# Kernel optimization log

Measured on AMD Instinct MI355X. Metric: run time of the kernel, lower is better.

## Reference

```python
import jax, jax.numpy as jnp
import numpy as np

B, C, T, F_ = 4, 128, 1000, 65
H, E, Dh = 4, 8, 32          # E = ceil(512/65), Dh = C // H
POOL, STRIDE = 10, 5
EPS = 1e-5


def setup_inputs() -> dict:
    key = jax.random.key(0)
    ks = jax.random.split(key, 16)
    s = 0.05
    d = {}
    d['batch'] = jax.random.normal(ks[0], (B, C, T, F_), jnp.float32)
    d['pos_cond'] = jax.random.normal(ks[1], (B, C, T, F_), jnp.float32)
    d['neg_cond'] = jax.random.normal(ks[2], (B, C, T, F_), jnp.float32)
    # per-head 1x1 conv params (stacked over heads), PReLU slopes, LN4DCF affine
    d['WQ'] = jax.random.normal(ks[3], (H, E, C), jnp.float32) * s
    d['bQ'] = jax.random.normal(ks[4], (H, E), jnp.float32) * s
    d['aQ'] = jnp.full((H,), 0.25, jnp.float32)
    d['gQ'] = jnp.ones((H, E, F_), jnp.float32)
    d['betQ'] = jnp.zeros((H, E, F_), jnp.float32)
    d['WK'] = jax.random.normal(ks[5], (H, E, C), jnp.float32) * s
    d['bK'] = jax.random.normal(ks[6], (H, E), jnp.float32) * s
    d['aK'] = jnp.full((H,), 0.25, jnp.float32)
    d['gK'] = jnp.ones((H, E, F_), jnp.float32)
    d['betK'] = jnp.zeros((H, E, F_), jnp.float32)
    d['WV'] = jax.random.normal(ks[7], (H, Dh, C), jnp.float32) * s
    d['bV'] = jax.random.normal(ks[8], (H, Dh), jnp.float32) * s
    d['aV'] = jnp.full((H,), 0.25, jnp.float32)
    d['gV'] = jnp.ones((H, Dh, F_), jnp.float32)
    d['betV'] = jnp.zeros((H, Dh, F_), jnp.float32)
    d['Wp'] = jax.random.normal(ks[9], (C, C), jnp.float32) * s
    d['bp'] = jax.random.normal(ks[10], (C,), jnp.float32) * s
    d['ap'] = jnp.full((1,), 0.25, jnp.float32)
    d['gp'] = jnp.ones((C, F_), jnp.float32)
    d['betp'] = jnp.zeros((C, F_), jnp.float32)
    return d


def _avg_pool_time(x):
    # x: [B, C, T, F] -> pool along T (torch pools after transposing to [.., F, T])
    xt = jnp.transpose(x, (0, 1, 3, 2))  # [B, C, F, T]
    y = jax.lax.reduce_window(xt, 0.0, jax.lax.add,
                              (1, 1, 1, POOL), (1, 1, 1, STRIDE), 'VALID') / POOL
    return jnp.transpose(y, (0, 1, 3, 2))  # [B, C, T', F]


def _head_branch(x, W, b, a, g, bet):
    # x: [B, Cin, Tx, F]; W: [H, Co, Cin] -> y: [H, B, Co, Tx, F]
    y = jnp.einsum('bctf,hec->hbetf', x, W) + b[:, None, :, None, None]
    y = jnp.where(y >= 0, y, a[:, None, None, None, None] * y)  # PReLU
    mu = jnp.mean(y, axis=(2, 4), keepdims=True)                 # LN over (C, F)
    var = jnp.var(y, axis=(2, 4), keepdims=True)
    return (y - mu) / jnp.sqrt(var + EPS) * g[:, None, :, None, :] + bet[:, None, :, None, :]


def reference(batch, pos_cond, neg_cond,
              WQ, bQ, aQ, gQ, betQ,
              WK, bK, aK, gK, betK,
              WV, bV, aV, gV, betV,
              Wp, bp, ap, gp, betp):
    cond = jnp.concatenate([_avg_pool_time(pos_cond), -_avg_pool_time(neg_cond)], axis=2)
    Tc = cond.shape[2]

    Q = _head_branch(batch, WQ, bQ, aQ, gQ, betQ)   # [H,B,E,T,F]
    K = _head_branch(cond, WK, bK, aK, gK, betK)    # [H,B,E,Tc,F]
    V = _head_branch(cond, WV, bV, aV, gV, betV)    # [H,B,Dh,Tc,F]

    Qf = jnp.transpose(Q, (0, 1, 3, 2, 4)).reshape(H, B, T, E * F_)
    Kf = jnp.transpose(K, (0, 1, 3, 2, 4)).reshape(H, B, Tc, E * F_)
    Vf = jnp.transpose(V, (0, 1, 3, 2, 4)).reshape(H, B, Tc, Dh * F_)

    scale = 1.0 / jnp.sqrt(jnp.float32(E * F_))
    attn = jax.nn.softmax(jnp.einsum('hbtd,hbsd->hbts', Qf, Kf) * scale, axis=-1)
    out = jnp.einsum('hbts,hbse->hbte', attn, Vf)   # [H,B,T,Dh*F]

    out = out.reshape(H, B, T, Dh, F_)
    out = jnp.transpose(out, (1, 0, 3, 2, 4)).reshape(B, C, T, F_)

    # concat projection: conv1x1 + PReLU + LN4DCF over (C, F)
    y = jnp.einsum('bctf,ec->betf', out, Wp) + bp[None, :, None, None]
    y = jnp.where(y >= 0, y, ap[0] * y)
    mu = jnp.mean(y, axis=(1, 3), keepdims=True)
    var = jnp.var(y, axis=(1, 3), keepdims=True)
    y = (y - mu) / jnp.sqrt(var + EPS) * gp[None, :, None, :] + betp[None, :, None, :]
    return y
```

## Files before the change

### kernel.cpp

```cpp
#include <hip/hip_runtime.h>
#include <hip/hip_bf16.h>

typedef unsigned short u16;
typedef __attribute__((ext_vector_type(8))) short bfrag;
typedef __attribute__((ext_vector_type(4))) float f32x4;

#define B_ 4
#define C_ 128
#define T_ 1000
#define F_ 65
#define H_ 4
#define E_ 8
#define DH_ 32
#define TP_ 199
#define TC_ 398
#define DQK 520
#define DQKP 544
#define DV 2080
#define SP_ 416
#define QROWS 1008
#define EPS 1e-5f

__device__ __forceinline__ float bf2f(u16 u) {
    union { float f; unsigned int i; } v; v.i = ((unsigned int)u) << 16; return v.f;
}
__device__ __forceinline__ u16 f2bf(float f) {
    union { float f; unsigned int i; } v; v.f = f;
    unsigned int x = v.i;
    return (u16)((x + 0x7FFFu + ((x >> 16) & 1u)) >> 16);
}

__device__ __forceinline__ float wred_sum(float v) {
#pragma unroll
    for (int o = 32; o > 0; o >>= 1) v += __shfl_down(v, o, 64);
    return __shfl(v, 0, 64);
}

__global__ __launch_bounds__(256)
void zerofill_kernel(uint4* __restrict__ dst, int n16) {
    int i = blockIdx.x * 256 + threadIdx.x;
    if (i < n16) dst[i] = make_uint4(0, 0, 0, 0);
}

__global__ __launch_bounds__(256)
void wconv3_kernel(const float* __restrict__ WQ, const float* __restrict__ WK,
                   const float* __restrict__ WV, u16* __restrict__ dst) {
    int i = blockIdx.x * 256 + threadIdx.x;
    if (i >= 24576) return;
    float v; int hipos, lopos;
    if (i < 4096)      { v = WQ[i];        hipos = i;        lopos = i + 4096;  }
    else if (i < 8192) { v = WK[i - 4096]; hipos = i + 4096; lopos = i + 8192;  }
    else               { v = WV[i - 8192]; hipos = i + 8192; lopos = i + 24576; }
    u16 hi = f2bf(v);
    dst[hipos] = hi;
    dst[lopos] = f2bf(v - bf2f(hi));
}

__global__ __launch_bounds__(256)
void pool_kernel(const float* __restrict__ pos, const float* __restrict__ neg,
                 u16* __restrict__ cond) {
    int idx = blockIdx.x * 256 + threadIdx.x;
    const int N = B_ * C_ * TC_ * F_;
    if (idx >= N) return;
    int f  = idx % F_;
    int tc = (idx / F_) % TC_;
    int c  = (idx / (F_ * TC_)) % C_;
    int b  = idx / (F_ * TC_ * C_);
    const float* src; float sign; int t0;
    if (tc < TP_) { src = pos; sign =  1.f; t0 = tc * 5; }
    else          { src = neg; sign = -1.f; t0 = (tc - TP_) * 5; }
    int base = ((b * C_ + c) * T_ + t0) * F_ + f;
    float s = 0.f;
#pragma unroll
    for (int k = 0; k < 10; k++) s += src[base + k * F_];
    cond[idx] = f2bf(s * (sign * 0.1f));
}

template <typename XT, bool SPLITX>
__global__ __launch_bounds__(256, 4)
void qk_mfma_kernel(const XT* __restrict__ x, int Tx, int rowsper, int ldout,
                    const u16* __restrict__ Wbf, const float* __restrict__ bias,
                    const float* __restrict__ alpha,
                    const float* __restrict__ g, const float* __restrict__ bet,
                    u16* __restrict__ out) {
    constexpr int XLO = 80 * 136;
    __shared__ u16 xt[(SPLITX ? 2 : 1) * 80 * 136];
    __shared__ float redS[8], redQ[8];
    int b = blockIdx.x / Tx, t = blockIdx.x % Tx;
    int tid = threadIdx.x;
    size_t xbase = (size_t)(b * C_) * Tx * F_ + (size_t)t * F_;
    for (int i = tid; i < C_ * F_; i += 256) {
        int c = i / F_, f = i % F_;
        if constexpr (SPLITX) {
            float v = (float)x[xbase + (size_t)c * Tx * F_ + f];
            u16 hi = f2bf(v);
            xt[f * 136 + c] = hi;
            xt[XLO + f * 136 + c] = f2bf(v - bf2f(hi));
        } else {
            xt[f * 136 + c] = (u16)x[xbase + (size_t)c * Tx * F_ + f];
        }
    }
    for (int i = tid; i < 15 * 128; i += 256) {
        xt[(65 + i / 128) * 136 + (i % 128)] = 0;
        if constexpr (SPLITX) xt[XLO + (65 + i / 128) * 136 + (i % 128)] = 0;
    }
    __syncthreads();

    int wave = tid >> 6, lane = tid & 63, gq = lane >> 4, n = lane & 15;
    int mt = wave & 1, fg = wave >> 1;
    int ftbase = fg ? 3 : 0;
    const int nft = 3;
    int jmax = fg ? 2 : 3;
    const u16* Wlo = Wbf + 32 * C_;
    f32x4 acc[3];
#pragma unroll
    for (int j = 0; j < nft; j++) acc[j] = (f32x4){0.f, 0.f, 0.f, 0.f};

    for (int c32 = 0; c32 < 4; c32++) {
        bfrag awh = *(const bfrag*)(Wbf + (size_t)(mt * 16 + n) * C_ + c32 * 32 + gq * 8);
        bfrag awl = *(const bfrag*)(Wlo + (size_t)(mt * 16 + n) * C_ + c32 * 32 + gq * 8);
#pragma unroll
        for (int j = 0; j < nft; j++) {
            if (j < jmax) {
                int boff = ((ftbase + j) * 16 + n) * 136 + c32 * 32 + gq * 8;
                bfrag bxh = *(const bfrag*)(&xt[boff]);
                acc[j] = __builtin_amdgcn_mfma_f32_16x16x32_bf16(awh, bxh, acc[j], 0, 0, 0);
                acc[j] = __builtin_amdgcn_mfma_f32_16x16x32_bf16(awl, bxh, acc[j], 0, 0, 0);
                if constexpr (SPLITX) {
                    bfrag bxl = *(const bfrag*)(&xt[XLO + boff]);
                    acc[j] = __builtin_amdgcn_mfma_f32_16x16x32_bf16(awh, bxl, acc[j], 0, 0, 0);
                }
            }
        }
    }

    int h = mt * 2 + (gq >> 1);
    int er0 = mt * 16 + gq * 4;
    float ap = alpha[h];
    float sum = 0.f, ss = 0.f;
#pragma unroll
    for (int j = 0; j < nft; j++) {
        if (j < jmax) {
#pragma unroll
            for (int r = 0; r < 4; r++) {
                float v = acc[j][r] + bias[er0 + r];
                v = (v >= 0.f) ? v : ap * v;
                acc[j][r] = v;
                int f = (ftbase + j) * 16 + n;
                if (f < F_) { sum += v; ss += v * v; }
            }
        }
    }
#pragma unroll
    for (int o = 1; o <= 8; o <<= 1) {
        sum += __shfl_xor(sum, o, 64);
        ss  += __shfl_xor(ss, o, 64);
    }
    sum += __shfl_xor(sum, 16, 64);
    ss  += __shfl_xor(ss, 16, 64);
    if (n == 0 && (gq & 1) == 0) { redS[h * 2 + fg] = sum; redQ[h * 2 + fg] = ss; }
    __syncthreads();
    float ts = redS[h * 2 + 0] + redS[h * 2 + 1];
    float tq = redQ[h * 2 + 0] + redQ[h * 2 + 1];
    float mu = ts * (1.f / 520.f);
    float var = tq * (1.f / 520.f) - mu * mu;
    float rs = rsqrtf(var + EPS);

    size_t obase = (size_t)((h * B_ + b) * rowsper + t) * ldout;
#pragma unroll
    for (int j = 0; j < nft; j++) {
        if (j < jmax) {
#pragma unroll
            for (int r = 0; r < 4; r++) {
                int f = (ftbase + j) * 16 + n;
                if (f < F_) {
                    int er = er0 + r;
                    int el = er & 7;
                    out[obase + el * F_ + f] =
                        f2bf((acc[j][r] - mu) * rs * g[er * F_ + f] + bet[er * F_ + f]);
                }
            }
        }
    }
}

__global__ __launch_bounds__(256, 4)
void v_mfma_kernel(const u16* __restrict__ x, const u16* __restrict__ Wbf,
                   const float* __restrict__ bias, const float* __restrict__ alpha,
                   const float* __restrict__ g, const float* __restrict__ bet,
                   u16* __restrict__ out) {
    __shared__ u16 xt[80 * 136];
    int b = blockIdx.x / TC_, t = blockIdx.x % TC_;
    int tid = threadIdx.x;
    size_t xbase = (size_t)(b * C_) * TC_ * F_ + (size_t)t * F_;
    for (int i = tid; i < C_ * F_; i += 256) {
        int c = i / F_, f = i % F_;
        xt[f * 136 + c] = x[xbase + (size_t)c * TC_ * F_ + f];
    }
    for (int i = tid; i < 15 * 128; i += 256)
        xt[(65 + i / 128) * 136 + (i % 128)] = 0;
    __syncthreads();

    int wave = tid >> 6, lane = tid & 63, gq = lane >> 4, n = lane & 15;
    const u16* Wlo = Wbf + 128 * C_;
    f32x4 acc[2][5];
#pragma unroll
    for (int a = 0; a < 2; a++)
#pragma unroll
        for (int ft = 0; ft < 5; ft++) acc[a][ft] = (f32x4){0.f, 0.f, 0.f, 0.f};

    for (int c32 = 0; c32 < 4; c32++) {
        bfrag aw0h = *(const bfrag*)(Wbf + (size_t)(wave * 32 + n) * C_ + c32 * 32 + gq * 8);
        bfrag aw0l = *(const bfrag*)(Wlo + (size_t)(wave * 32 + n) * C_ + c32 * 32 + gq * 8);
        bfrag aw1h = *(const bfrag*)(Wbf + (size_t)(wave * 32 + 16 + n) * C_ + c32 * 32 + gq * 8);
        bfrag aw1l = *(const bfrag*)(Wlo + (size_t)(wave * 32 + 16 + n) * C_ + c32 * 32 + gq * 8);
#pragma unroll
        for (int ft = 0; ft < 5; ft++) {
            bfrag bx = *(const bfrag*)(&xt[(ft * 16 + n) * 136 + c32 * 32 + gq * 8]);
            acc[0][ft] = __builtin_amdgcn_mfma_f32_16x16x32_bf16(aw0h, bx, acc[0][ft], 0, 0, 0);
            acc[0][ft] = __builtin_amdgcn_mfma_f32_16x16x32_bf16(aw0l, bx, acc[0][ft], 0, 0, 0);
            acc[1][ft] = __builtin_amdgcn_mfma_f32_16x16x32_bf16(aw1h, bx, acc[1][ft], 0, 0, 0);
            acc[1][ft] = __builtin_amdgcn_mfma_f32_16x16x32_bf16(aw1l, bx, acc[1][ft], 0, 0, 0);
        }
    }

    int h = wave;
    float ap = alpha[h];
    float sum = 0.f, ss = 0.f;
#pragma unroll
    for (int a = 0; a < 2; a++) {
        int er0 = wave * 32 + a * 16 + gq * 4;
#pragma unroll
        for (int r = 0; r < 4; r++) {
            float bb = bias[er0 + r];
#pragma unroll
            for (int ft = 0; ft < 5; ft++) {
                float v = acc[a][ft][r] + bb;
                v = (v >= 0.f) ? v : ap * v;
                acc[a][ft][r] = v;
                int f = ft * 16 + n;
                if (f < F_) { sum += v; ss += v * v; }
            }
        }
    }
    sum = wred_sum(sum); ss = wred_sum(ss);
    float mu = sum * (1.f / 2080.f);
    float var = ss * (1.f / 2080.f) - mu * mu;
    float rs = rsqrtf(var + EPS);

    size_t obase = (size_t)((h * B_ + b) * TC_ + t) * DV;
#pragma unroll
    for (int a = 0; a < 2; a++) {
#pragma unroll
        for (int r = 0; r < 4; r++) {
            int er = wave * 32 + a * 16 + gq * 4 + r;
            int drow = er & 31;
#pragma unroll
            for (int ft = 0; ft < 5; ft++) {
                int f = ft * 16 + n;
                if (f < F_) {
                    out[obase + drow * F_ + f] =
                        f2bf((acc[a][ft][r] - mu) * rs * g[er * F_ + f] + bet[er * F_ + f]);
                }
            }
        }
    }
}

__global__ __launch_bounds__(256)
void transpose_v_kernel(const u16* __restrict__ Vf, u16* __restrict__ Vt) {
    __shared__ u16 tileb[32][33];
    int id = blockIdx.x;
    int sb = id % 13; id /= 13;
    int eb = id % 65; int hb = id / 65;
    const u16* src = Vf + (size_t)hb * TC_ * DV;
    u16* dst = Vt + (size_t)hb * DV * SP_;
    int j = threadIdx.x & 31, i0 = threadIdx.x >> 5;
#pragma unroll
    for (int k = 0; k < 4; k++) {
        int i = i0 + 8 * k;
        int s = sb * 32 + i, e = eb * 32 + j;
        u16 v = 0;
        if (s < TC_) v = src[(size_t)s * DV + e];
        tileb[i][j] = v;
    }
    __syncthreads();
#pragma unroll
    for (int k = 0; k < 4; k++) {
        int i2 = i0 + 8 * k;
        int e = eb * 32 + i2, s = sb * 32 + j;
        dst[(size_t)e * SP_ + s] = tileb[j][i2];
    }
}

__global__ __launch_bounds__(256, 4)
void attn_kernel(const u16* __restrict__ Qf, const u16* __restrict__ Kf,
                 const u16* __restrict__ Vt, float* __restrict__ out) {
    __shared__ u16 qlds[16 * 552];
    __shared__ u16 plds[16 * 424];
    __shared__ float redmax[16 * 4];
    __shared__ float redsum[16 * 4];

    int tile = blockIdx.x % 63;
    int hb   = blockIdx.x / 63;
    int h = hb >> 2, b = hb & 3;
    int tid = threadIdx.x;
    int wave = tid >> 6, lane = tid & 63;
    int g = lane >> 4;
    int n = lane & 15;
    int tq0 = tile * 16;

    const u16* qbase = Qf + (size_t)(hb * QROWS + tq0) * DQK;
    for (int i = tid; i < 16 * 69; i += 256) {
        int q = i / 69, cb = i % 69;
        uint4 val = make_uint4(0, 0, 0, 0);
        if (cb < 65) val = *(const uint4*)(qbase + (size_t)q * DQK + cb * 8);
        *(uint4*)(&qlds[q * 552 + cb * 8]) = val;
    }
    __syncthreads();

    f32x4 acc[7];
#pragma unroll
    for (int i = 0; i < 7; i++) acc[i] = (f32x4){0.f, 0.f, 0.f, 0.f};
    const u16* kslab = Kf + (size_t)hb * SP_ * DQKP;
    for (int c = 0; c < 17; c++) {
        bfrag aq = *(const bfrag*)(&qlds[n * 552 + c * 32 + g * 8]);
#pragma unroll
        for (int i = 0; i < 7; i++) {
            int tau = wave + 4 * i;
            if (tau < 26) {
                bfrag bk = *(const bfrag*)(kslab + (size_t)(tau * 16 + n) * DQKP + c * 32 + g * 8);
                acc[i] = __builtin_amdgcn_mfma_f32_16x16x32_bf16(aq, bk, acc[i], 0, 0, 0);
            }
        }
    }

    const float scale = 0.043852900965f;
    float m4[4], s4[4];
#pragma unroll
    for (int r = 0; r < 4; r++) {
        float mx = -1e30f;
#pragma unroll
        for (int i = 0; i < 7; i++) {
            int tau = wave + 4 * i;
            int s = tau * 16 + n;
            if (tau < 26 && s < TC_) mx = fmaxf(mx, acc[i][r] * scale);
        }
        mx = fmaxf(mx, __shfl_xor(mx, 1, 64));
        mx = fmaxf(mx, __shfl_xor(mx, 2, 64));
        mx = fmaxf(mx, __shfl_xor(mx, 4, 64));
        mx = fmaxf(mx, __shfl_xor(mx, 8, 64));
        m4[r] = mx;
    }
    if (n == 0) {
#pragma unroll
        for (int r = 0; r < 4; r++) redmax[(g * 4 + r) * 4 + wave] = m4[r];
    }
    __syncthreads();
#pragma unroll
    for (int r = 0; r < 4; r++) {
        int q = g * 4 + r;
        m4[r] = fmaxf(fmaxf(redmax[q * 4 + 0], redmax[q * 4 + 1]),
                      fmaxf(redmax[q * 4 + 2], redmax[q * 4 + 3]));
        s4[r] = 0.f;
    }
#pragma unroll
    for (int i = 0; i < 7; i++) {
        int tau = wave + 4 * i;
        if (tau < 26) {
            int s = tau * 16 + n;
#pragma unroll
            for (int r = 0; r < 4; r++) {
                float e = (s < TC_) ? __expf(acc[i][r] * scale - m4[r]) : 0.f;
                acc[i][r] = e;
                s4[r] += e;
            }
        }
    }
#pragma unroll
    for (int r = 0; r < 4; r++) {
        float sm = s4[r];
        sm += __shfl_xor(sm, 1, 64);
        sm += __shfl_xor(sm, 2, 64);
        sm += __shfl_xor(sm, 4, 64);
        sm += __shfl_xor(sm, 8, 64);
        s4[r] = sm;
    }
    if (n == 0) {
#pragma unroll
        for (int r = 0; r < 4; r++) redsum[(g * 4 + r) * 4 + wave] = s4[r];
    }
    __syncthreads();
#pragma unroll
    for (int r = 0; r < 4; r++) {
        int q = g * 4 + r;
        float tot = redsum[q * 4 + 0] + redsum[q * 4 + 1] + redsum[q * 4 + 2] + redsum[q * 4 + 3];
        s4[r] = 1.0f / tot;
    }
#pragma unroll
    for (int i = 0; i < 7; i++) {
        int tau = wave + 4 * i;
        if (tau < 26) {
            int s = tau * 16 + n;
#pragma unroll
            for (int r = 0; r < 4; r++) {
                plds[(g * 4 + r) * 424 + s] = f2bf(acc[i][r] * s4[r]);
            }
        }
    }
    __syncthreads();

    bfrag bp[13];
#pragma unroll
    for (int c = 0; c < 13; c++)
        bp[c] = *(const bfrag*)(&plds[n * 424 + c * 32 + g * 8]);

    const u16* vslab = Vt + (size_t)hb * DV * SP_;
    int t = tq0 + n;
    for (int j = 0; j < 17; j++) {
        int p = wave + 4 * j;
        if (p >= 65) break;
        int e0 = p * 32;
        f32x4 a0 = (f32x4){0.f, 0.f, 0.f, 0.f};
        f32x4 a1 = (f32x4){0.f, 0.f, 0.f, 0.f};
#pragma unroll
        for (int c = 0; c < 13; c++) {
            bfrag v0 = *(const bfrag*)(vslab + (size_t)(e0 + n) * SP_ + c * 32 + g * 8);
            bfrag v1 = *(const bfrag*)(vslab + (size_t)(e0 + 16 + n) * SP_ + c * 32 + g * 8);
            a0 = __builtin_amdgcn_mfma_f32_16x16x32_bf16(v0, bp[c], a0, 0, 0, 0);
            a1 = __builtin_amdgcn_mfma_f32_16x16x32_bf16(v1, bp[c], a1, 0, 0, 0);
        }
        if (t < T_) {
#pragma unroll
            for (int r = 0; r < 4; r++) {
                int e = e0 + g * 4 + r;
                int dh = e / F_, f = e - dh * F_;
                out[((size_t)(b * C_ + h * DH_ + dh) * T_ + t) * F_ + f] = a0[r];
                int e2 = e0 + 16 + g * 4 + r;
                int dh2 = e2 / F_, f2 = e2 - dh2 * F_;
                out[((size_t)(b * C_ + h * DH_ + dh2) * T_ + t) * F_ + f2] = a1[r];
            }
        }
    }
}

__global__ __launch_bounds__(256)
void wconv_kernel(const float* __restrict__ W, u16* __restrict__ Wbf) {
    int i = blockIdx.x * 256 + threadIdx.x;
    if (i < C_ * C_) {
        float v = W[i];
        u16 hi = f2bf(v);
        Wbf[i] = hi;
        Wbf[C_ * C_ + i] = f2bf(v - bf2f(hi));
    }
}

__global__ __launch_bounds__(256, 4)
void proj_mfma_kernel(float* __restrict__ io, const u16* __restrict__ Wbf,
                      const float* __restrict__ bpr, const float* __restrict__ apr,
                      const float* __restrict__ gpr, const float* __restrict__ betpr) {
    __shared__ u16 xt[80 * 136];
    __shared__ float wsum[4], wss[4];
    int b = blockIdx.x / T_, t = blockIdx.x % T_;
    int tid = threadIdx.x;
    size_t xbase = (size_t)(b * C_) * T_ * F_ + (size_t)t * F_;

    for (int i = tid; i < C_ * F_; i += 256) {
        int c = i / F_, f = i % F_;
        xt[f * 136 + c] = f2bf(io[xbase + (size_t)c * T_ * F_ + f]);
    }
    for (int i = tid; i < 15 * 128; i += 256) {
        int f = 65 + i / 128, c = i % 128;
        xt[f * 136 + c] = 0;
    }
    __syncthreads();

    int wave = tid >> 6, lane = tid & 63, g = lane >> 4, n = lane & 15;
    const u16* Wlo = Wbf + C_ * C_;
    f32x4 acc[2][5];
#pragma unroll
    for (int a = 0; a < 2; a++)
#pragma unroll
        for (int ft = 0; ft < 5; ft++) acc[a][ft] = (f32x4){0.f, 0.f, 0.f, 0.f};

    for (int c32 = 0; c32 < 4; c32++) {
        bfrag aw0h = *(const bfrag*)(Wbf + (size_t)(wave * 32 + n) * C_ + c32 * 32 + g * 8);
        bfrag aw0l = *(const bfrag*)(Wlo + (size_t)(wave * 32 + n) * C_ + c32 * 32 + g * 8);
        bfrag aw1h = *(const bfrag*)(Wbf + (size_t)(wave * 32 + 16 + n) * C_ + c32 * 32 + g * 8);
        bfrag aw1l = *(const bfrag*)(Wlo + (size_t)(wave * 32 + 16 + n) * C_ + c32 * 32 + g * 8);
#pragma unroll
        for (int ft = 0; ft < 5; ft++) {
            bfrag bx = *(const bfrag*)(&xt[(ft * 16 + n) * 136 + c32 * 32 + g * 8]);
            acc[0][ft] = __builtin_amdgcn_mfma_f32_16x16x32_bf16(aw0h, bx, acc[0][ft], 0, 0, 0);
            acc[0][ft] = __builtin_amdgcn_mfma_f32_16x16x32_bf16(aw0l, bx, acc[0][ft], 0, 0, 0);
            acc[1][ft] = __builtin_amdgcn_mfma_f32_16x16x32_bf16(aw1h, bx, acc[1][ft], 0, 0, 0);
            acc[1][ft] = __builtin_amdgcn_mfma_f32_16x16x32_bf16(aw1l, bx, acc[1][ft], 0, 0, 0);
        }
    }

    float a_p = apr[0];
    float sum = 0.f, ss = 0.f;
#pragma unroll
    for (int a = 0; a < 2; a++) {
        int e0 = wave * 32 + a * 16 + g * 4;
#pragma unroll
        for (int r = 0; r < 4; r++) {
            float bb = bpr[e0 + r];
#pragma unroll
            for (int ft = 0; ft < 5; ft++) {
                float v = acc[a][ft][r] + bb;
                v = (v >= 0.f) ? v : a_p * v;
                acc[a][ft][r] = v;
                int f = ft * 16 + n;
                if (f < F_) { sum += v; ss += v * v; }
            }
        }
    }
    sum = wred_sum(sum); ss = wred_sum(ss);
    if (lane == 0) { wsum[wave] = sum; wss[wave] = ss; }
    __syncthreads();
    float tsum = wsum[0] + wsum[1] + wsum[2] + wsum[3];
    float tss  = wss[0] + wss[1] + wss[2] + wss[3];
    float mu = tsum * (1.f / 8320.f);
    float var = tss * (1.f / 8320.f) - mu * mu;
    float rs = rsqrtf(var + EPS);

#pragma unroll
    for (int a = 0; a < 2; a++) {
#pragma unroll
        for (int r = 0; r < 4; r++) {
            int e = wave * 32 + a * 16 + g * 4 + r;
#pragma unroll
            for (int ft = 0; ft < 5; ft++) {
                int f = ft * 16 + n;
                if (f < F_) {
                    io[((size_t)(b * C_ + e) * T_ + t) * F_ + f] =
                        (acc[a][ft][r] - mu) * rs * gpr[e * F_ + f] + betpr[e * F_ + f];
                }
            }
        }
    }
}

extern "C" void kernel_launch(void* const* d_in, const int* in_sizes, int n_in,
                              void* d_out, int out_size, void* d_ws, size_t ws_size,
                              hipStream_t stream) {
    const float* batch = (const float*)d_in[0];
    const float* pos   = (const float*)d_in[1];
    const float* neg   = (const float*)d_in[2];
    const float* WQ   = (const float*)d_in[3];
    const float* bQ   = (const float*)d_in[4];
    const float* aQ   = (const float*)d_in[5];
    const float* gQ   = (const float*)d_in[6];
    const float* betQ = (const float*)d_in[7];
    const float* WK   = (const float*)d_in[8];
    const float* bK   = (const float*)d_in[9];
    const float* aK   = (const float*)d_in[10];
    const float* gK   = (const float*)d_in[11];
    const float* betK = (const float*)d_in[12];
    const float* WV   = (const float*)d_in[13];
    const float* bV   = (const float*)d_in[14];
    const float* aV   = (const float*)d_in[15];
    const float* gV   = (const float*)d_in[16];
    const float* betV = (const float*)d_in[17];
    const float* Wp   = (const float*)d_in[18];
    const float* bp   = (const float*)d_in[19];
    const float* ap   = (const float*)d_in[20];
    const float* gp   = (const float*)d_in[21];
    const float* betp = (const float*)d_in[22];

    char* ws = (char*)d_ws;
    u16* Vt   = (u16*)(ws);
    u16* cond = (u16*)(ws);
    u16* Wqkv = (u16*)(ws + 26490880);
    u16* Qf   = (u16*)(ws + 27688960);
    u16* Kf   = (u16*)(ws + 44462080);
    u16* Vf   = (u16*)(ws + 51703808);
    u16* Wpbf = (u16*)(ws + 51703808);
    u16* WQbf = Wqkv;
    u16* WKbf = Wqkv + 8192;
    u16* WVbf = Wqkv + 16384;
    float* o  = (float*)d_out;

    wconv3_kernel<<<96, 256, 0, stream>>>(WQ, WK, WV, Wqkv);
    const int NPOOL = B_ * C_ * TC_ * F_;
    pool_kernel<<<(NPOOL + 255) / 256, 256, 0, stream>>>(pos, neg, cond);
    const int KF16 = (16 * SP_ * DQKP * 2) / 16;
    zerofill_kernel<<<(KF16 + 255) / 256, 256, 0, stream>>>((uint4*)Kf, KF16);
    qk_mfma_kernel<float, true><<<B_ * T_,  256, 0, stream>>>(batch, T_,  QROWS, DQK,  WQbf, bQ, aQ, gQ, betQ, Qf);
    qk_mfma_kernel<u16, false> <<<B_ * TC_, 256, 0, stream>>>(cond,  TC_, SP_,   DQKP, WKbf, bK, aK, gK, betK, Kf);
    v_mfma_kernel<<<B_ * TC_, 256, 0, stream>>>(cond, WVbf, bV, aV, gV, betV, Vf);
    transpose_v_kernel<<<16 * 65 * 13, 256, 0, stream>>>(Vf, Vt);
    wconv_kernel<<<(C_ * C_ + 255) / 256, 256, 0, stream>>>(Wp, Wpbf);
    attn_kernel<<<16 * 63, 256, 0, stream>>>(Qf, Kf, Vt, o);
    proj_mfma_kernel<<<B_ * T_, 256, 0, stream>>>(o, Wpbf, bp, ap, gp, betp);
}
```

Baseline: 894.8 us.

## Process 32 query rows per attention block and pre-swizzle V into MFMA fragment layout

The attention kernel now handles two 16-row query tiles per block, so each V fragment loaded from global memory feeds two MFMAs and block count halves. The V transpose kernel now writes V directly in per-lane MFMA fragment order, so each lane reads contiguous 16-byte chunks. This is meant to cut V traffic and uncoalesced loads in attention. In exchange, register pressure rises (launch bounds lowered to 3), the grid drops to 512 blocks with some padded rows, and K is still reloaded once per query tile.

```diff
diff --git a/kernel.cpp b/kernel.cpp
--- a/kernel.cpp
+++ b/kernel.cpp
@@ -19,6 +19,7 @@
 #define DV 2080
 #define SP_ 416
 #define QROWS 1008
+#define VTP 13312
 #define EPS 1e-5f
 
 __device__ __forceinline__ float bf2f(u16 u) {
@@ -269,176 +270,209 @@
 
 __global__ __launch_bounds__(256)
 void transpose_v_kernel(const u16* __restrict__ Vf, u16* __restrict__ Vt) {
-    __shared__ u16 tileb[32][33];
-    int id = blockIdx.x;
-    int sb = id % 13; id /= 13;
-    int eb = id % 65; int hb = id / 65;
-    const u16* src = Vf + (size_t)hb * TC_ * DV;
-    u16* dst = Vt + (size_t)hb * DV * SP_;
-    int j = threadIdx.x & 31, i0 = threadIdx.x >> 5;
-#pragma unroll
-    for (int k = 0; k < 4; k++) {
-        int i = i0 + 8 * k;
-        int s = sb * 32 + i, e = eb * 32 + j;
-        u16 v = 0;
-        if (s < TC_) v = src[(size_t)s * DV + e];
-        tileb[i][j] = v;
-    }
-    __syncthreads();
-#pragma unroll
-    for (int k = 0; k < 4; k++) {
-        int i2 = i0 + 8 * k;
-        int e = eb * 32 + i2, s = sb * 32 + j;
-        dst[(size_t)e * SP_ + s] = tileb[j][i2];
-    }
-}
-
-__global__ __launch_bounds__(256, 4)
+    __shared__ u16 tile[32 * 424];
+    int p  = blockIdx.x % 65;
+    int hb = blockIdx.x / 65;
+    const u16* src = Vf + (size_t)hb * TC_ * DV + p * 32;
+    u16* dst = Vt + ((size_t)hb * 65 + p) * VTP;
+    int tid = threadIdx.x;
+    for (int i = tid; i < 416 * 32; i += 256) {
+        int e = i & 31, s = i >> 5;
+        tile[e * 424 + s] = (s < TC_) ? src[(size_t)s * DV + e] : (u16)0;
+    }
+    __syncthreads();
+    for (int k = tid; k < 1664; k += 256) {
+        int c = k >> 7, r = k & 127;
+        int eh = r >> 6, l = r & 63;
+        int nn = l & 15, gg = l >> 4;
+        uint4 val = *(const uint4*)(&tile[(eh * 16 + nn) * 424 + c * 32 + gg * 8]);
+        *(uint4*)(&dst[(size_t)k * 8]) = val;
+    }
+}
+
+__global__ __launch_bounds__(256, 3)
 void attn_kernel(const u16* __restrict__ Qf, const u16* __restrict__ Kf,
                  const u16* __restrict__ Vt, float* __restrict__ out) {
-    __shared__ u16 qlds[16 * 552];
-    __shared__ u16 plds[16 * 424];
-    __shared__ float redmax[16 * 4];
-    __shared__ float redsum[16 * 4];
-
-    int tile = blockIdx.x % 63;
-    int hb   = blockIdx.x / 63;
+    __shared__ u16 shbuf[32 * 424];
+    __shared__ float redmax[32 * 4];
+    __shared__ float redsum[32 * 4];
+
+    int tile = blockIdx.x & 31;
+    int hb   = blockIdx.x >> 5;
     int h = hb >> 2, b = hb & 3;
     int tid = threadIdx.x;
     int wave = tid >> 6, lane = tid & 63;
     int g = lane >> 4;
     int n = lane & 15;
-    int tq0 = tile * 16;
-
-    const u16* qbase = Qf + (size_t)(hb * QROWS + tq0) * DQK;
-    for (int i = tid; i < 16 * 69; i += 256) {
-        int q = i / 69, cb = i % 69;
-        uint4 val = make_uint4(0, 0, 0, 0);
-        if (cb < 65) val = *(const uint4*)(qbase + (size_t)q * DQK + cb * 8);
-        *(uint4*)(&qlds[q * 552 + cb * 8]) = val;
-    }
-    __syncthreads();
-
-    f32x4 acc[7];
-#pragma unroll
-    for (int i = 0; i < 7; i++) acc[i] = (f32x4){0.f, 0.f, 0.f, 0.f};
+    int tq0 = tile * 32;
+
     const u16* kslab = Kf + (size_t)hb * SP_ * DQKP;
-    for (int c = 0; c < 17; c++) {
-        bfrag aq = *(const bfrag*)(&qlds[n * 552 + c * 32 + g * 8]);
-#pragma unroll
-        for (int i = 0; i < 7; i++) {
-            int tau = wave + 4 * i;
-            if (tau < 26) {
-                bfrag bk = *(const bfrag*)(kslab + (size_t)(tau * 16 + n) * DQKP + c * 32 + g * 8);
-                acc[i] = __builtin_amdgcn_mfma_f32_16x16x32_bf16(aq, bk, acc[i], 0, 0, 0);
-            }
-        }
+    const u16* qbase = Qf + (size_t)hb * QROWS * DQK;
+
+    f32x4 acc[2][7];
+#pragma unroll
+    for (int qt = 0; qt < 2; qt++)
+#pragma unroll
+        for (int i = 0; i < 7; i++) acc[qt][i] = (f32x4){0.f, 0.f, 0.f, 0.f};
+
+#pragma unroll
+    for (int qt = 0; qt < 2; qt++) {
+        for (int i = tid; i < 16 * 69; i += 256) {
+            int q = i / 69, cb = i % 69;
+            int qg = tq0 + qt * 16 + q;
+            uint4 val = make_uint4(0, 0, 0, 0);
+            if (qg < QROWS && cb < 65)
+                val = *(const uint4*)(qbase + (size_t)qg * DQK + cb * 8);
+            *(uint4*)(&shbuf[q * 552 + cb * 8]) = val;
+        }
+        __syncthreads();
+        for (int c = 0; c < 17; c++) {
+            bfrag aq = *(const bfrag*)(&shbuf[n * 552 + c * 32 + g * 8]);
+#pragma unroll
+            for (int i = 0; i < 7; i++) {
+                int tau = wave + 4 * i;
+                if (tau < 26) {
+                    bfrag bk = *(const bfrag*)(kslab + (size_t)(tau * 16 + n) * DQKP + c * 32 + g * 8);
+                    acc[qt][i] = __builtin_amdgcn_mfma_f32_16x16x32_bf16(aq, bk, acc[qt][i], 0, 0, 0);
+                }
+            }
+        }
+        __syncthreads();
     }
 
     const float scale = 0.043852900965f;
-    float m4[4], s4[4];
-#pragma unroll
-    for (int r = 0; r < 4; r++) {
-        float mx = -1e30f;
-#pragma unroll
-        for (int i = 0; i < 7; i++) {
-            int tau = wave + 4 * i;
-            int s = tau * 16 + n;
-            if (tau < 26 && s < TC_) mx = fmaxf(mx, acc[i][r] * scale);
-        }
-        mx = fmaxf(mx, __shfl_xor(mx, 1, 64));
-        mx = fmaxf(mx, __shfl_xor(mx, 2, 64));
-        mx = fmaxf(mx, __shfl_xor(mx, 4, 64));
-        mx = fmaxf(mx, __shfl_xor(mx, 8, 64));
-        m4[r] = mx;
+    float m4[2][4], s4[2][4];
+#pragma unroll
+    for (int qt = 0; qt < 2; qt++) {
+#pragma unroll
+        for (int r = 0; r < 4; r++) {
+            float mx = -1e30f;
+#pragma unroll
+            for (int i = 0; i < 7; i++) {
+                int tau = wave + 4 * i;
+                int s = tau * 16 + n;
+                if (tau < 26 && s < TC_) mx = fmaxf(mx, acc[qt][i][r] * scale);
+            }
+            mx = fmaxf(mx, __shfl_xor(mx, 1, 64));
+            mx = fmaxf(mx, __shfl_xor(mx, 2, 64));
+            mx = fmaxf(mx, __shfl_xor(mx, 4, 64));
+            mx = fmaxf(mx, __shfl_xor(mx, 8, 64));
+            m4[qt][r] = mx;
+        }
     }
     if (n == 0) {
 #pragma unroll
-        for (int r = 0; r < 4; r++) redmax[(g * 4 + r) * 4 + wave] = m4[r];
-    }
-    __syncthreads();
-#pragma unroll
-    for (int r = 0; r < 4; r++) {
-        int q = g * 4 + r;
-        m4[r] = fmaxf(fmaxf(redmax[q * 4 + 0], redmax[q * 4 + 1]),
-                      fmaxf(redmax[q * 4 + 2], redmax[q * 4 + 3]));
-        s4[r] = 0.f;
-    }
+        for (int qt = 0; qt < 2; qt++)
+#pragma unroll
+            for (int r = 0; r < 4; r++)
+                redmax[(qt * 16 + g * 4 + r) * 4 + wave] = m4[qt][r];
+    }
+    __syncthreads();
+#pragma unroll
+    for (int qt = 0; qt < 2; qt++)
+#pragma unroll
+        for (int r = 0; r < 4; r++) {
+            int q = qt * 16 + g * 4 + r;
+            m4[qt][r] = fmaxf(fmaxf(redmax[q * 4 + 0], redmax[q * 4 + 1]),
+                              fmaxf(redmax[q * 4 + 2], redmax[q * 4 + 3]));
+            s4[qt][r] = 0.f;
+        }
 #pragma unroll
     for (int i = 0; i < 7; i++) {
         int tau = wave + 4 * i;
         if (tau < 26) {
             int s = tau * 16 + n;
 #pragma unroll
-            for (int r = 0; r < 4; r++) {
-                float e = (s < TC_) ? __expf(acc[i][r] * scale - m4[r]) : 0.f;
-                acc[i][r] = e;
-                s4[r] += e;
-            }
-        }
-    }
-#pragma unroll
-    for (int r = 0; r < 4; r++) {
-        float sm = s4[r];
-        sm += __shfl_xor(sm, 1, 64);
-        sm += __shfl_xor(sm, 2, 64);
-        sm += __shfl_xor(sm, 4, 64);
-        sm += __shfl_xor(sm, 8, 64);
-        s4[r] = sm;
-    }
+            for (int qt = 0; qt < 2; qt++)
+#pragma unroll
+                for (int r = 0; r < 4; r++) {
+                    float e = (s < TC_) ? __expf(acc[qt][i][r] * scale - m4[qt][r]) : 0.f;
+                    acc[qt][i][r] = e;
+                    s4[qt][r] += e;
+                }
+        }
+    }
+#pragma unroll
+    for (int qt = 0; qt < 2; qt++)
+#pragma unroll
+        for (int r = 0; r < 4; r++) {
+            float sm = s4[qt][r];
+            sm += __shfl_xor(sm, 1, 64);
+            sm += __shfl_xor(sm, 2, 64);
+            sm += __shfl_xor(sm, 4, 64);
+            sm += __shfl_xor(sm, 8, 64);
+            s4[qt][r] = sm;
+        }
     if (n == 0) {
 #pragma unroll
-        for (int r = 0; r < 4; r++) redsum[(g * 4 + r) * 4 + wave] = s4[r];
-    }
-    __syncthreads();
-#pragma unroll
-    for (int r = 0; r < 4; r++) {
-        int q = g * 4 + r;
-        float tot = redsum[q * 4 + 0] + redsum[q * 4 + 1] + redsum[q * 4 + 2] + redsum[q * 4 + 3];
-        s4[r] = 1.0f / tot;
-    }
+        for (int qt = 0; qt < 2; qt++)
+#pragma unroll
+            for (int r = 0; r < 4; r++)
+                redsum[(qt * 16 + g * 4 + r) * 4 + wave] = s4[qt][r];
+    }
+    __syncthreads();
+#pragma unroll
+    for (int qt = 0; qt < 2; qt++)
+#pragma unroll
+        for (int r = 0; r < 4; r++) {
+            int q = qt * 16 + g * 4 + r;
+            float tot = redsum[q * 4 + 0] + redsum[q * 4 + 1] +
+                        redsum[q * 4 + 2] + redsum[q * 4 + 3];
+            s4[qt][r] = 1.0f / tot;
+        }
 #pragma unroll
     for (int i = 0; i < 7; i++) {
         int tau = wave + 4 * i;
         if (tau < 26) {
             int s = tau * 16 + n;
 #pragma unroll
-            for (int r = 0; r < 4; r++) {
-                plds[(g * 4 + r) * 424 + s] = f2bf(acc[i][r] * s4[r]);
-            }
-        }
-    }
-    __syncthreads();
-
-    bfrag bp[13];
-#pragma unroll
-    for (int c = 0; c < 13; c++)
-        bp[c] = *(const bfrag*)(&plds[n * 424 + c * 32 + g * 8]);
-
-    const u16* vslab = Vt + (size_t)hb * DV * SP_;
-    int t = tq0 + n;
+            for (int qt = 0; qt < 2; qt++)
+#pragma unroll
+                for (int r = 0; r < 4; r++)
+                    shbuf[(qt * 16 + g * 4 + r) * 424 + s] = f2bf(acc[qt][i][r] * s4[qt][r]);
+        }
+    }
+    __syncthreads();
+
+    bfrag bp[2][13];
+#pragma unroll
+    for (int qt = 0; qt < 2; qt++)
+#pragma unroll
+        for (int c = 0; c < 13; c++)
+            bp[qt][c] = *(const bfrag*)(&shbuf[(qt * 16 + n) * 424 + c * 32 + g * 8]);
+
+    const u16* vslab = Vt + (size_t)hb * 65 * VTP;
     for (int j = 0; j < 17; j++) {
         int p = wave + 4 * j;
         if (p >= 65) break;
+        const u16* vb = vslab + (size_t)p * VTP + lane * 8;
+        f32x4 a00 = (f32x4){0.f,0.f,0.f,0.f}, a01 = (f32x4){0.f,0.f,0.f,0.f};
+        f32x4 a10 = (f32x4){0.f,0.f,0.f,0.f}, a11 = (f32x4){0.f,0.f,0.f,0.f};
+#pragma unroll
+        for (int c = 0; c < 13; c++) {
+            bfrag v0 = *(const bfrag*)(vb + c * 1024);
+            bfrag v1 = *(const bfrag*)(vb + c * 1024 + 512);
+            a00 = __builtin_amdgcn_mfma_f32_16x16x32_bf16(v0, bp[0][c], a00, 0, 0, 0);
+            a01 = __builtin_amdgcn_mfma_f32_16x16x32_bf16(v0, bp[1][c], a01, 0, 0, 0);
+            a10 = __builtin_amdgcn_mfma_f32_16x16x32_bf16(v1, bp[0][c], a10, 0, 0, 0);
+            a11 = __builtin_amdgcn_mfma_f32_16x16x32_bf16(v1, bp[1][c], a11, 0, 0, 0);
+        }
         int e0 = p * 32;
-        f32x4 a0 = (f32x4){0.f, 0.f, 0.f, 0.f};
-        f32x4 a1 = (f32x4){0.f, 0.f, 0.f, 0.f};
-#pragma unroll
-        for (int c = 0; c < 13; c++) {
-            bfrag v0 = *(const bfrag*)(vslab + (size_t)(e0 + n) * SP_ + c * 32 + g * 8);
-            bfrag v1 = *(const bfrag*)(vslab + (size_t)(e0 + 16 + n) * SP_ + c * 32 + g * 8);
-            a0 = __builtin_amdgcn_mfma_f32_16x16x32_bf16(v0, bp[c], a0, 0, 0, 0);
-            a1 = __builtin_amdgcn_mfma_f32_16x16x32_bf16(v1, bp[c], a1, 0, 0, 0);
-        }
-        if (t < T_) {
-#pragma unroll
-            for (int r = 0; r < 4; r++) {
-                int e = e0 + g * 4 + r;
-                int dh = e / F_, f = e - dh * F_;
-                out[((size_t)(b * C_ + h * DH_ + dh) * T_ + t) * F_ + f] = a0[r];
-                int e2 = e0 + 16 + g * 4 + r;
-                int dh2 = e2 / F_, f2 = e2 - dh2 * F_;
-                out[((size_t)(b * C_ + h * DH_ + dh2) * T_ + t) * F_ + f2] = a1[r];
+#pragma unroll
+        for (int qt = 0; qt < 2; qt++) {
+            int t = tq0 + qt * 16 + n;
+            if (t < T_) {
+#pragma unroll
+                for (int r = 0; r < 4; r++) {
+                    int e = e0 + g * 4 + r;
+                    int dh = e / F_, f = e - dh * F_;
+                    float v0w = qt ? a01[r] : a00[r];
+                    out[((size_t)(b * C_ + h * DH_ + dh) * T_ + t) * F_ + f] = v0w;
+                    int e2 = e0 + 16 + g * 4 + r;
+                    int dh2 = e2 / F_, f2 = e2 - dh2 * F_;
+                    float v1w = qt ? a11[r] : a10[r];
+                    out[((size_t)(b * C_ + h * DH_ + dh2) * T_ + t) * F_ + f2] = v1w;
+                }
             }
         }
     }
@@ -590,8 +624,8 @@
     qk_mfma_kernel<float, true><<<B_ * T_,  256, 0, stream>>>(batch, T_,  QROWS, DQK,  WQbf, bQ, aQ, gQ, betQ, Qf);
     qk_mfma_kernel<u16, false> <<<B_ * TC_, 256, 0, stream>>>(cond,  TC_, SP_,   DQKP, WKbf, bK, aK, gK, betK, Kf);
     v_mfma_kernel<<<B_ * TC_, 256, 0, stream>>>(cond, WVbf, bV, aV, gV, betV, Vf);
-    transpose_v_kernel<<<16 * 65 * 13, 256, 0, stream>>>(Vf, Vt);
+    transpose_v_kernel<<<16 * 65, 256, 0, stream>>>(Vf, Vt);
     wconv_kernel<<<(C_ * C_ + 255) / 256, 256, 0, stream>>>(Wp, Wpbf);
-    attn_kernel<<<16 * 63, 256, 0, stream>>>(Qf, Kf, Vt, o);
+    attn_kernel<<<16 * 32, 256, 0, stream>>>(Qf, Kf, Vt, o);
     proj_mfma_kernel<<<B_ * T_, 256, 0, stream>>>(o, Wpbf, bp, ap, gp, betp);
 }
```

Measured after the change: 868.0 us. 3.0% less time.
